# Kernel tuning notes

Measured on AMD Instinct MI355X. Metric: run time of the kernel, lower is better.

## Reference

```python
import jax, jax.numpy as jnp
import numpy as np

N_NODES = 50000
N_EDGES = 800000
NUM_FEAT = 96
DIM = 64


def _mean_aggregate(x, src, tgt, num_nodes):
    # gather source-node features along edges, sum into targets, divide by in-degree
    msgs = x[src]  # [E, F] irregular gather
    summed = jax.ops.segment_sum(msgs, tgt, num_segments=num_nodes)  # [N, F]
    cnt = jax.ops.segment_sum(jnp.ones((src.shape[0],), x.dtype), tgt, num_segments=num_nodes)
    return summed / jnp.maximum(cnt, 1.0)[:, None]


def _sage_conv(x, src, tgt, W_l, W_r, b):
    # PyG SAGEConv: lin_l(mean_{j in N(i)} x_j) + lin_r(x_i) + bias
    aggr = _mean_aggregate(x, src, tgt, x.shape[0])
    return aggr @ W_l + x @ W_r + b


def setup_inputs() -> dict:
    key = jax.random.key(0)
    ks = jax.random.split(key, 8)
    x = jax.random.normal(ks[0], (N_NODES, NUM_FEAT), dtype=jnp.float32)
    edge_index = jax.random.randint(ks[1], (2, N_EDGES), 0, N_NODES, dtype=jnp.int32)
    s = 0.05
    Wl1 = jax.random.normal(ks[2], (NUM_FEAT, DIM), dtype=jnp.float32) * s
    Wr1 = jax.random.normal(ks[3], (NUM_FEAT, DIM), dtype=jnp.float32) * s
    b1 = jnp.zeros((DIM,), dtype=jnp.float32)
    Wl2 = jax.random.normal(ks[4], (DIM, DIM), dtype=jnp.float32) * s
    Wr2 = jax.random.normal(ks[5], (DIM, DIM), dtype=jnp.float32) * s
    b2 = jnp.zeros((DIM,), dtype=jnp.float32)
    return {"x": x, "edge_index": edge_index, "Wl1": Wl1, "Wr1": Wr1, "b1": b1,
            "Wl2": Wl2, "Wr2": Wr2, "b2": b2}


def reference(x, edge_index, Wl1, Wr1, b1, Wl2, Wr2, b2):
    src, tgt = edge_index[0], edge_index[1]
    h = jax.nn.relu(_sage_conv(x, src, tgt, Wl1, Wr1, b1))
    # F.dropout(..., training=self.training): evaluated in eval mode -> identity
    out = _sage_conv(h, src, tgt, Wl2, Wr2, b2)
    return out
```

## Files before the change

### kernel.cpp

```cpp
#include <hip/hip_runtime.h>
#include <hip/hip_bf16.h>

#define NFEAT 96
#define DIM 64

template <int K>
__global__ __launch_bounds__(256) void k_mm_hist(const float* __restrict__ X,
                                                 const float* __restrict__ Wl,
                                                 const float* __restrict__ Wr,
                                                 const float* __restrict__ b,
                                                 __hip_bfloat16* __restrict__ A,
                                                 __hip_bfloat16* __restrict__ B, int N,
                                                 const int* __restrict__ tgt,
                                                 int* __restrict__ cnt, int E,
                                                 int part_size, int mmB) {
    constexpr int ROWS = 32;
    __shared__ float xs[ROWS * K];
    const int t = threadIdx.x;

    if ((int)blockIdx.x >= mmB) {
        const int part = blockIdx.x & 7;
        const int hb = blockIdx.x - mmB;
        const int q = hb >> 3;
        const int nq = (gridDim.x - mmB) >> 3;
        const int stride = nq * blockDim.x;
        for (int i = q * blockDim.x + t; i < E; i += stride) {
            const int tg = tgt[i];
            if (tg / part_size == part) atomicAdd(&cnt[tg], 1);
        }
        return;
    }

    const int lane = t & 63;
    const int w = t >> 6;
    const int r0 = blockIdx.x * ROWS;
    const int nvalid = min(ROWS, N - r0);

    if (nvalid > 0) {
        const float4* src = reinterpret_cast<const float4*>(X + (size_t)r0 * K);
        float4* dst = reinterpret_cast<float4*>(xs);
        const int nv4 = (nvalid * K) >> 2;
        for (int c = t; c < nv4; c += 256) dst[c] = src[c];
    }
    const float bias = b[lane];
    __syncthreads();
    if (nvalid <= 0) return;

    const int rw = w * 8;
    float accl[8], accr[8];
#pragma unroll
    for (int i = 0; i < 8; ++i) { accl[i] = 0.f; accr[i] = 0.f; }

    for (int k = 0; k < K; k += 4) {
        const float wl0 = Wl[(k + 0) * DIM + lane];
        const float wl1 = Wl[(k + 1) * DIM + lane];
        const float wl2 = Wl[(k + 2) * DIM + lane];
        const float wl3 = Wl[(k + 3) * DIM + lane];
        const float wr0 = Wr[(k + 0) * DIM + lane];
        const float wr1 = Wr[(k + 1) * DIM + lane];
        const float wr2 = Wr[(k + 2) * DIM + lane];
        const float wr3 = Wr[(k + 3) * DIM + lane];
#pragma unroll
        for (int i = 0; i < 8; ++i) {
            const float4 xv = *reinterpret_cast<const float4*>(&xs[(rw + i) * K + k]);
            accl[i] = fmaf(xv.x, wl0, accl[i]);
            accl[i] = fmaf(xv.y, wl1, accl[i]);
            accl[i] = fmaf(xv.z, wl2, accl[i]);
            accl[i] = fmaf(xv.w, wl3, accl[i]);
            accr[i] = fmaf(xv.x, wr0, accr[i]);
            accr[i] = fmaf(xv.y, wr1, accr[i]);
            accr[i] = fmaf(xv.z, wr2, accr[i]);
            accr[i] = fmaf(xv.w, wr3, accr[i]);
        }
    }
#pragma unroll
    for (int i = 0; i < 8; ++i) {
        const int r = r0 + rw + i;
        if (r < N) {
            A[(size_t)r * DIM + lane] = __float2bfloat16(accl[i]);
            B[(size_t)r * DIM + lane] = __float2bfloat16(accr[i] + bias);
        }
    }
}

template <int K>
__global__ __launch_bounds__(256) void k_mm(const float* __restrict__ X,
                                            const float* __restrict__ Wl,
                                            const float* __restrict__ Wr,
                                            const float* __restrict__ b,
                                            __hip_bfloat16* __restrict__ A,
                                            __hip_bfloat16* __restrict__ B, int N) {
    constexpr int ROWS = 32;
    __shared__ float xs[ROWS * K];
    const int t = threadIdx.x;
    const int lane = t & 63;
    const int w = t >> 6;
    const int r0 = blockIdx.x * ROWS;
    const int nvalid = min(ROWS, N - r0);

    {
        const float4* src = reinterpret_cast<const float4*>(X + (size_t)r0 * K);
        float4* dst = reinterpret_cast<float4*>(xs);
        const int nv4 = (nvalid * K) >> 2;
        for (int c = t; c < nv4; c += 256) dst[c] = src[c];
    }
    const float bias = b[lane];
    __syncthreads();

    const int rw = w * 8;
    float accl[8], accr[8];
#pragma unroll
    for (int i = 0; i < 8; ++i) { accl[i] = 0.f; accr[i] = 0.f; }

    for (int k = 0; k < K; k += 4) {
        const float wl0 = Wl[(k + 0) * DIM + lane];
        const float wl1 = Wl[(k + 1) * DIM + lane];
        const float wl2 = Wl[(k + 2) * DIM + lane];
        const float wl3 = Wl[(k + 3) * DIM + lane];
        const float wr0 = Wr[(k + 0) * DIM + lane];
        const float wr1 = Wr[(k + 1) * DIM + lane];
        const float wr2 = Wr[(k + 2) * DIM + lane];
        const float wr3 = Wr[(k + 3) * DIM + lane];
#pragma unroll
        for (int i = 0; i < 8; ++i) {
            const float4 xv = *reinterpret_cast<const float4*>(&xs[(rw + i) * K + k]);
            accl[i] = fmaf(xv.x, wl0, accl[i]);
            accl[i] = fmaf(xv.y, wl1, accl[i]);
            accl[i] = fmaf(xv.z, wl2, accl[i]);
            accl[i] = fmaf(xv.w, wl3, accl[i]);
            accr[i] = fmaf(xv.x, wr0, accr[i]);
            accr[i] = fmaf(xv.y, wr1, accr[i]);
            accr[i] = fmaf(xv.z, wr2, accr[i]);
            accr[i] = fmaf(xv.w, wr3, accr[i]);
        }
    }
#pragma unroll
    for (int i = 0; i < 8; ++i) {
        const int r = r0 + rw + i;
        if (r < N) {
            A[(size_t)r * DIM + lane] = __float2bfloat16(accl[i]);
            B[(size_t)r * DIM + lane] = __float2bfloat16(accr[i] + bias);
        }
    }
}


__global__ void k_scan1(const int* __restrict__ cnt, int* __restrict__ bsum, int N) {
    __shared__ int ws[4];
    const int t = threadIdx.x;
    const int lane = t & 63, w = t >> 6;
    const int base = blockIdx.x * 1024 + t * 4;
    int s = 0;
    if (base + 3 < N) {
        int4 v = *reinterpret_cast<const int4*>(cnt + base);
        s = v.x + v.y + v.z + v.w;
    } else {
        for (int i = 0; i < 4; ++i)
            if (base + i < N) s += cnt[base + i];
    }
    for (int off = 32; off; off >>= 1) s += __shfl_down(s, off, 64);
    if (lane == 0) ws[w] = s;
    __syncthreads();
    if (t == 0) bsum[blockIdx.x] = ws[0] + ws[1] + ws[2] + ws[3];
}

__global__ void k_scan2(const int* __restrict__ bsum, int* __restrict__ boff,
                        int* __restrict__ rowstart, int nb, int N) {
    const int lane = threadIdx.x;
    int carry = 0;
    for (int b0 = 0; b0 < nb; b0 += 64) {
        int i = b0 + lane;
        int orig = (i < nb) ? bsum[i] : 0;
        int v = orig;
        for (int off = 1; off < 64; off <<= 1) {
            int u = __shfl_up(v, off, 64);
            if (lane >= off) v += u;
        }
        if (i < nb) boff[i] = carry + v - orig;
        carry += __shfl(v, 63, 64);
    }
    if (lane == 0) rowstart[N] = carry;
}

__global__ void k_scan3(const int* __restrict__ cnt, const int* __restrict__ boff,
                        int* __restrict__ rowstart, int* __restrict__ wpos, int N) {
    __shared__ int wsum[4];
    const int t = threadIdx.x;
    const int lane = t & 63, w = t >> 6;
    const int base = blockIdx.x * 1024 + t * 4;
    int4 v = make_int4(0, 0, 0, 0);
    if (base + 3 < N) {
        v = *reinterpret_cast<const int4*>(cnt + base);
    } else {
        int* p = &v.x;
        for (int i = 0; i < 4; ++i)
            if (base + i < N) p[i] = cnt[base + i];
    }
    const int s = v.x + v.y + v.z + v.w;
    int inc = s;
    for (int off = 1; off < 64; off <<= 1) {
        int u = __shfl_up(inc, off, 64);
        if (lane >= off) inc += u;
    }
    if (lane == 63) wsum[w] = inc;
    __syncthreads();
    int woff = 0;
    for (int i = 0; i < w; ++i) woff += wsum[i];
    int r = boff[blockIdx.x] + woff + inc - s;
    if (base + 0 < N) { rowstart[base + 0] = r; wpos[base + 0] = r; } r += v.x;
    if (base + 1 < N) { rowstart[base + 1] = r; wpos[base + 1] = r; } r += v.y;
    if (base + 2 < N) { rowstart[base + 2] = r; wpos[base + 2] = r; } r += v.z;
    if (base + 3 < N) { rowstart[base + 3] = r; wpos[base + 3] = r; }
}

__global__ void k_scatter(const int* __restrict__ src, const int* __restrict__ tgt,
                          int* __restrict__ wpos, int* __restrict__ csr_src, int E,
                          int part_size) {
    const int part = blockIdx.x & 7;
    const int q = blockIdx.x >> 3;
    const int nq = gridDim.x >> 3;
    const int stride = nq * blockDim.x;
    for (int i = q * blockDim.x + threadIdx.x; i < E; i += stride) {
        const int tg = tgt[i];
        if (tg / part_size == part) {
            const int p = atomicAdd(&wpos[tg], 1);
            csr_src[p] = src[i];
        }
    }
}

template <bool RELU>
__global__ void k_aggr(const __hip_bfloat16* __restrict__ A,
                       const __hip_bfloat16* __restrict__ Bm,
                       const int* __restrict__ rowstart, const int* __restrict__ csr_src,
                       float* __restrict__ out, int N) {
    const int lane = threadIdx.x & 63;
    const int wave = blockIdx.x * (blockDim.x >> 6) + (threadIdx.x >> 6);
    const int nwaves = gridDim.x * (blockDim.x >> 6);
    for (int n = wave; n < N; n += nwaves) {
        const int r0 = rowstart[n];
        const int r1 = rowstart[n + 1];
        float s0 = 0.f, s1 = 0.f, s2 = 0.f, s3 = 0.f;
        int j = r0;
        for (; j + 3 < r1; j += 4) {
            const int c0 = csr_src[j];
            const int c1 = csr_src[j + 1];
            const int c2 = csr_src[j + 2];
            const int c3 = csr_src[j + 3];
            s0 += __bfloat162float(A[(size_t)c0 * DIM + lane]);
            s1 += __bfloat162float(A[(size_t)c1 * DIM + lane]);
            s2 += __bfloat162float(A[(size_t)c2 * DIM + lane]);
            s3 += __bfloat162float(A[(size_t)c3 * DIM + lane]);
        }
        for (; j < r1; ++j) s0 += __bfloat162float(A[(size_t)csr_src[j] * DIM + lane]);
        const float c = (float)(r1 - r0);
        float v = ((s0 + s1) + (s2 + s3)) / fmaxf(c, 1.f) +
                  __bfloat162float(Bm[(size_t)n * DIM + lane]);
        if (RELU) v = fmaxf(v, 0.f);
        out[(size_t)n * DIM + lane] = v;
    }
}

extern "C" void kernel_launch(void* const* d_in, const int* in_sizes, int n_in,
                              void* d_out, int out_size, void* d_ws, size_t ws_size,
                              hipStream_t stream) {
    const float* x   = (const float*)d_in[0];
    const int*   ei  = (const int*)d_in[1];
    const float* Wl1 = (const float*)d_in[2];
    const float* Wr1 = (const float*)d_in[3];
    const float* b1  = (const float*)d_in[4];
    const float* Wl2 = (const float*)d_in[5];
    const float* Wr2 = (const float*)d_in[6];
    const float* b2  = (const float*)d_in[7];
    float* out = (float*)d_out;

    const int N = in_sizes[0] / NFEAT;
    const int E = in_sizes[1] / 2;
    const int* src = ei;
    const int* tgt = ei + E;

    char* ws = (char*)d_ws;
    size_t off = 0;
    auto alloc = [&](size_t bytes) -> void* {
        void* p = ws + off;
        off = (off + bytes + 255) & ~(size_t)255;
        return p;
    };
    const int nb = (N + 1023) / 1024;
    int*   cnt      = (int*)alloc((size_t)N * 4);
    int*   rowstart = (int*)alloc((size_t)(N + 1) * 4);
    int*   wpos     = (int*)alloc((size_t)N * 4);
    int*   bsum     = (int*)alloc((size_t)nb * 4);
    int*   boff     = (int*)alloc((size_t)nb * 4);
    int*   csr      = (int*)alloc((size_t)E * 4);
    __hip_bfloat16* A = (__hip_bfloat16*)alloc((size_t)N * DIM * 2);
    __hip_bfloat16* B = (__hip_bfloat16*)alloc((size_t)N * DIM * 2);
    float* H        = (float*)alloc((size_t)N * DIM * 4);

    hipMemsetAsync(cnt, 0, (size_t)N * 4, stream);

    const int part_size = (N + 7) / 8;
    const int mm_blocks = (N + 31) / 32;
    const int mmB = (mm_blocks + 7) & ~7;
    const int histB = 2048;

    k_mm_hist<NFEAT><<<mmB + histB, 256, 0, stream>>>(x, Wl1, Wr1, b1, A, B, N,
                                                      tgt, cnt, E, part_size, mmB);
    k_scan1<<<nb, 256, 0, stream>>>(cnt, bsum, N);
    k_scan2<<<1, 64, 0, stream>>>(bsum, boff, rowstart, nb, N);
    k_scan3<<<nb, 256, 0, stream>>>(cnt, boff, rowstart, wpos, N);
    k_scatter<<<2048, 256, 0, stream>>>(src, tgt, wpos, csr, E, part_size);

    k_aggr<true><<<2048, 256, 0, stream>>>(A, B, rowstart, csr, H, N);

    k_mm<DIM><<<mm_blocks, 256, 0, stream>>>(H, Wl2, Wr2, b2, A, B, N);
    k_aggr<false><<<2048, 256, 0, stream>>>(A, B, rowstart, csr, out, N);
}
```

Measured before the change: 264.8 us.

## Fuse layer-1 aggregation into layer-2 projection and vectorize edge loads

Result: slower. 308.8 us (+16.6%).

```diff
diff --git a/kernel.cpp b/kernel.cpp
--- a/kernel.cpp
+++ b/kernel.cpp
@@ -23,9 +23,17 @@
         const int hb = blockIdx.x - mmB;
         const int q = hb >> 3;
         const int nq = (gridDim.x - mmB) >> 3;
-        const int stride = nq * blockDim.x;
-        for (int i = q * blockDim.x + t; i < E; i += stride) {
-            const int tg = tgt[i];
+        const int step = nq * blockDim.x * 4;
+        const int E4 = E & ~3;
+        for (int i = (q * blockDim.x + t) * 4; i < E4; i += step) {
+            const int4 tv = *reinterpret_cast<const int4*>(tgt + i);
+            if (tv.x / part_size == part) atomicAdd(&cnt[tv.x], 1);
+            if (tv.y / part_size == part) atomicAdd(&cnt[tv.y], 1);
+            if (tv.z / part_size == part) atomicAdd(&cnt[tv.z], 1);
+            if (tv.w / part_size == part) atomicAdd(&cnt[tv.w], 1);
+        }
+        if (q == 0 && t < (E - E4)) {
+            const int tg = tgt[E4 + t];
             if (tg / part_size == part) atomicAdd(&cnt[tg], 1);
         }
         return;
@@ -45,67 +53,6 @@
     const float bias = b[lane];
     __syncthreads();
     if (nvalid <= 0) return;
-
-    const int rw = w * 8;
-    float accl[8], accr[8];
-#pragma unroll
-    for (int i = 0; i < 8; ++i) { accl[i] = 0.f; accr[i] = 0.f; }
-
-    for (int k = 0; k < K; k += 4) {
-        const float wl0 = Wl[(k + 0) * DIM + lane];
-        const float wl1 = Wl[(k + 1) * DIM + lane];
-        const float wl2 = Wl[(k + 2) * DIM + lane];
-        const float wl3 = Wl[(k + 3) * DIM + lane];
-        const float wr0 = Wr[(k + 0) * DIM + lane];
-        const float wr1 = Wr[(k + 1) * DIM + lane];
-        const float wr2 = Wr[(k + 2) * DIM + lane];
-        const float wr3 = Wr[(k + 3) * DIM + lane];
-#pragma unroll
-        for (int i = 0; i < 8; ++i) {
-            const float4 xv = *reinterpret_cast<const float4*>(&xs[(rw + i) * K + k]);
-            accl[i] = fmaf(xv.x, wl0, accl[i]);
-            accl[i] = fmaf(xv.y, wl1, accl[i]);
-            accl[i] = fmaf(xv.z, wl2, accl[i]);
-            accl[i] = fmaf(xv.w, wl3, accl[i]);
-            accr[i] = fmaf(xv.x, wr0, accr[i]);
-            accr[i] = fmaf(xv.y, wr1, accr[i]);
-            accr[i] = fmaf(xv.z, wr2, accr[i]);
-            accr[i] = fmaf(xv.w, wr3, accr[i]);
-        }
-    }
-#pragma unroll
-    for (int i = 0; i < 8; ++i) {
-        const int r = r0 + rw + i;
-        if (r < N) {
-            A[(size_t)r * DIM + lane] = __float2bfloat16(accl[i]);
-            B[(size_t)r * DIM + lane] = __float2bfloat16(accr[i] + bias);
-        }
-    }
-}
-
-template <int K>
-__global__ __launch_bounds__(256) void k_mm(const float* __restrict__ X,
-                                            const float* __restrict__ Wl,
-                                            const float* __restrict__ Wr,
-                                            const float* __restrict__ b,
-                                            __hip_bfloat16* __restrict__ A,
-                                            __hip_bfloat16* __restrict__ B, int N) {
-    constexpr int ROWS = 32;
-    __shared__ float xs[ROWS * K];
-    const int t = threadIdx.x;
-    const int lane = t & 63;
-    const int w = t >> 6;
-    const int r0 = blockIdx.x * ROWS;
-    const int nvalid = min(ROWS, N - r0);
-
-    {
-        const float4* src = reinterpret_cast<const float4*>(X + (size_t)r0 * K);
-        float4* dst = reinterpret_cast<float4*>(xs);
-        const int nv4 = (nvalid * K) >> 2;
-        for (int c = t; c < nv4; c += 256) dst[c] = src[c];
-    }
-    const float bias = b[lane];
-    __syncthreads();
 
     const int rw = w * 8;
     float accl[8], accr[8];
@@ -219,21 +166,108 @@
     const int part = blockIdx.x & 7;
     const int q = blockIdx.x >> 3;
     const int nq = gridDim.x >> 3;
-    const int stride = nq * blockDim.x;
-    for (int i = q * blockDim.x + threadIdx.x; i < E; i += stride) {
-        const int tg = tgt[i];
-        if (tg / part_size == part) {
-            const int p = atomicAdd(&wpos[tg], 1);
-            csr_src[p] = src[i];
-        }
-    }
-}
-
-template <bool RELU>
-__global__ void k_aggr(const __hip_bfloat16* __restrict__ A,
-                       const __hip_bfloat16* __restrict__ Bm,
-                       const int* __restrict__ rowstart, const int* __restrict__ csr_src,
-                       float* __restrict__ out, int N) {
+    const int step = nq * blockDim.x * 4;
+    const int E4 = E & ~3;
+    for (int i = (q * blockDim.x + threadIdx.x) * 4; i < E4; i += step) {
+        const int4 tv = *reinterpret_cast<const int4*>(tgt + i);
+        const int4 sv = *reinterpret_cast<const int4*>(src + i);
+        if (tv.x / part_size == part) csr_src[atomicAdd(&wpos[tv.x], 1)] = sv.x;
+        if (tv.y / part_size == part) csr_src[atomicAdd(&wpos[tv.y], 1)] = sv.y;
+        if (tv.z / part_size == part) csr_src[atomicAdd(&wpos[tv.z], 1)] = sv.z;
+        if (tv.w / part_size == part) csr_src[atomicAdd(&wpos[tv.w], 1)] = sv.w;
+    }
+    if (q == 0 && threadIdx.x < (E - E4)) {
+        const int e = E4 + threadIdx.x;
+        const int tg = tgt[e];
+        if (tg / part_size == part) csr_src[atomicAdd(&wpos[tg], 1)] = src[e];
+    }
+}
+
+__global__ __launch_bounds__(256) void k_aggr_mm(const __hip_bfloat16* __restrict__ A1,
+                                                 const __hip_bfloat16* __restrict__ B1,
+                                                 const int* __restrict__ rowstart,
+                                                 const int* __restrict__ csr_src,
+                                                 const float* __restrict__ Wl,
+                                                 const float* __restrict__ Wr,
+                                                 const float* __restrict__ b,
+                                                 __hip_bfloat16* __restrict__ A2,
+                                                 __hip_bfloat16* __restrict__ B2, int N) {
+    constexpr int K = DIM;
+    __shared__ float xs[32 * K];
+    const int t = threadIdx.x;
+    const int lane = t & 63;
+    const int w = t >> 6;
+    const int r0 = blockIdx.x * 32;
+
+    for (int kq = 0; kq < 8; ++kq) {
+        const int n = r0 + w * 8 + kq;
+        float v = 0.f;
+        if (n < N) {
+            const int e0 = rowstart[n];
+            const int e1 = rowstart[n + 1];
+            float s0 = 0.f, s1 = 0.f, s2 = 0.f, s3 = 0.f;
+            int j = e0;
+            for (; j + 3 < e1; j += 4) {
+                const int c0 = csr_src[j];
+                const int c1 = csr_src[j + 1];
+                const int c2 = csr_src[j + 2];
+                const int c3 = csr_src[j + 3];
+                s0 += __bfloat162float(A1[(size_t)c0 * DIM + lane]);
+                s1 += __bfloat162float(A1[(size_t)c1 * DIM + lane]);
+                s2 += __bfloat162float(A1[(size_t)c2 * DIM + lane]);
+                s3 += __bfloat162float(A1[(size_t)c3 * DIM + lane]);
+            }
+            for (; j < e1; ++j) s0 += __bfloat162float(A1[(size_t)csr_src[j] * DIM + lane]);
+            v = ((s0 + s1) + (s2 + s3)) / fmaxf((float)(e1 - e0), 1.f) +
+                __bfloat162float(B1[(size_t)n * DIM + lane]);
+            v = fmaxf(v, 0.f);
+        }
+        xs[(w * 8 + kq) * K + lane] = v;
+    }
+    const float bias = b[lane];
+    __syncthreads();
+
+    const int rw = w * 8;
+    float accl[8], accr[8];
+#pragma unroll
+    for (int i = 0; i < 8; ++i) { accl[i] = 0.f; accr[i] = 0.f; }
+
+    for (int k = 0; k < K; k += 4) {
+        const float wl0 = Wl[(k + 0) * DIM + lane];
+        const float wl1 = Wl[(k + 1) * DIM + lane];
+        const float wl2 = Wl[(k + 2) * DIM + lane];
+        const float wl3 = Wl[(k + 3) * DIM + lane];
+        const float wr0 = Wr[(k + 0) * DIM + lane];
+        const float wr1 = Wr[(k + 1) * DIM + lane];
+        const float wr2 = Wr[(k + 2) * DIM + lane];
+        const float wr3 = Wr[(k + 3) * DIM + lane];
+#pragma unroll
+        for (int i = 0; i < 8; ++i) {
+            const float4 xv = *reinterpret_cast<const float4*>(&xs[(rw + i) * K + k]);
+            accl[i] = fmaf(xv.x, wl0, accl[i]);
+            accl[i] = fmaf(xv.y, wl1, accl[i]);
+            accl[i] = fmaf(xv.z, wl2, accl[i]);
+            accl[i] = fmaf(xv.w, wl3, accl[i]);
+            accr[i] = fmaf(xv.x, wr0, accr[i]);
+            accr[i] = fmaf(xv.y, wr1, accr[i]);
+            accr[i] = fmaf(xv.z, wr2, accr[i]);
+            accr[i] = fmaf(xv.w, wr3, accr[i]);
+        }
+    }
+#pragma unroll
+    for (int i = 0; i < 8; ++i) {
+        const int r = r0 + rw + i;
+        if (r < N) {
+            A2[(size_t)r * DIM + lane] = __float2bfloat16(accl[i]);
+            B2[(size_t)r * DIM + lane] = __float2bfloat16(accr[i] + bias);
+        }
+    }
+}
+
+__global__ void k_aggr_out(const __hip_bfloat16* __restrict__ A,
+                           const __hip_bfloat16* __restrict__ Bm,
+                           const int* __restrict__ rowstart, const int* __restrict__ csr_src,
+                           float* __restrict__ out, int N) {
     const int lane = threadIdx.x & 63;
     const int wave = blockIdx.x * (blockDim.x >> 6) + (threadIdx.x >> 6);
     const int nwaves = gridDim.x * (blockDim.x >> 6);
@@ -254,10 +288,8 @@
         }
         for (; j < r1; ++j) s0 += __bfloat162float(A[(size_t)csr_src[j] * DIM + lane]);
         const float c = (float)(r1 - r0);
-        float v = ((s0 + s1) + (s2 + s3)) / fmaxf(c, 1.f) +
-                  __bfloat162float(Bm[(size_t)n * DIM + lane]);
-        if (RELU) v = fmaxf(v, 0.f);
-        out[(size_t)n * DIM + lane] = v;
+        out[(size_t)n * DIM + lane] = ((s0 + s1) + (s2 + s3)) / fmaxf(c, 1.f) +
+                                      __bfloat162float(Bm[(size_t)n * DIM + lane]);
     }
 }
 
@@ -295,7 +327,8 @@
     int*   csr      = (int*)alloc((size_t)E * 4);
     __hip_bfloat16* A = (__hip_bfloat16*)alloc((size_t)N * DIM * 2);
     __hip_bfloat16* B = (__hip_bfloat16*)alloc((size_t)N * DIM * 2);
-    float* H        = (float*)alloc((size_t)N * DIM * 4);
+    __hip_bfloat16* A2 = (__hip_bfloat16*)alloc((size_t)N * DIM * 2);
+    __hip_bfloat16* B2 = (__hip_bfloat16*)alloc((size_t)N * DIM * 2);
 
     hipMemsetAsync(cnt, 0, (size_t)N * 4, stream);
 
@@ -311,8 +344,8 @@
     k_scan3<<<nb, 256, 0, stream>>>(cnt, boff, rowstart, wpos, N);
     k_scatter<<<2048, 256, 0, stream>>>(src, tgt, wpos, csr, E, part_size);
 
-    k_aggr<true><<<2048, 256, 0, stream>>>(A, B, rowstart, csr, H, N);
-
-    k_mm<DIM><<<mm_blocks, 256, 0, stream>>>(H, Wl2, Wr2, b2, A, B, N);
-    k_aggr<false><<<2048, 256, 0, stream>>>(A, B, rowstart, csr, out, N);
-}
+    k_aggr_mm<<<mm_blocks, 256, 0, stream>>>(A, B, rowstart, csr,
+                                             Wl2, Wr2, b2, A2, B2, N);
+
+    k_aggr_out<<<2048, 256, 0, stream>>>(A2, B2, rowstart, csr, out, N);
+}
```
